# Optimization experiments

Measured on AMD Instinct MI355X. Metric: run time of the kernel, lower is better.

## Reference

```python
import jax, jax.numpy as jnp
import numpy as np

G, NP, DEG = 2, 332, 32            # graphs, ROIs per graph (AAL-332), out-degree
INDIM, D1, D2, D3, NCLASS = 332, 332, 332, 128, 2
KH, R = 6, 332                      # edge-weight-MLP bottleneck, ROI one-hot dim
K1, K2 = 166, 83                    # ceil(0.5*332), ceil(0.5*166)
N, E = G * NP, G * NP * DEG
NEG, EPS = -1e9, 1e-5


def _seg_softmax(logits, seg, n):
    m = jax.ops.segment_max(logits, seg, num_segments=n)
    e = jnp.exp(logits - m[seg])
    return e / jax.ops.segment_sum(e, seg, num_segments=n)[seg]


def _conv(xv, src, dst, eattr, emask, posv, W1, W2, nb, b, out_dim):
    # MyNNConv: per-node weight matrix from pos via tiny MLP, then
    # x' = x @ W_node, messages weighted by softmax(edge_weight) per target.
    n, din = xv.shape
    w = (jnp.maximum(posv @ W1, 0.0) @ W2 + nb).reshape(n, din, out_dim)
    xt = jnp.einsum('ni,nio->no', xv, w)
    sl = jnp.arange(n, dtype=src.dtype)                 # self loops, weight 1
    s2 = jnp.concatenate([src, sl])
    d2 = jnp.concatenate([dst, sl])
    logit = jnp.concatenate([jnp.where(emask, eattr, NEG), jnp.ones((n,), xv.dtype)])
    alpha = _seg_softmax(logit, d2, n)
    return jax.ops.segment_sum(alpha[:, None] * xt[s2], d2, num_segments=n) + b


def _pool(xv, src, dst, emask, w, g, n_per, k):
    # TopKPooling(multiplier=1, nonlinearity=sigmoid)
    score = jax.nn.sigmoid((xv @ w) / jnp.linalg.norm(w))
    _, idx = jax.lax.top_k(score.reshape(g, n_per), k)
    perm = (idx + jnp.arange(g)[:, None] * n_per).reshape(-1)
    x_new = xv[perm] * score[perm][:, None]
    newidx = jnp.full((g * n_per,), -1, jnp.int32).at[perm].set(jnp.arange(g * k, dtype=jnp.int32))
    ns, nd = newidx[src], newidx[dst]
    m = emask & (ns >= 0) & (nd >= 0)                   # edges with both ends kept
    return x_new, jnp.where(m, ns, 0), jnp.where(m, nd, 0), m, perm


def _readout(xv, seg, g, cnt):
    mx = jax.ops.segment_max(xv, seg, num_segments=g)
    mn = jax.ops.segment_sum(xv, seg, num_segments=g) / cnt
    return jnp.concatenate([mx, mn], axis=1)


def _bn(xv, gm, bt):
    return (xv - xv.mean(0)) / jnp.sqrt(xv.var(0) + EPS) * gm + bt


def _forward(edge_index, x, edge_attr, pos,
             conv1_W1, conv1_W2, conv1_nb, conv1_b, pool1_w,
             conv2_W1, conv2_W2, conv2_nb, conv2_b, pool2_w,
             fc1_W, fc1_b, bn1_g, bn1_b, fc2_W, fc2_b, bn2_g, bn2_b, fc3_W, fc3_b):
    src, dst = edge_index[0], edge_index[1]
    emask = jnp.ones((E,), bool)
    h = _conv(x, src, dst, edge_attr, emask, pos, conv1_W1, conv1_W2, conv1_nb, conv1_b, D1)
    h, src, dst, emask, perm1 = _pool(h, src, dst, emask, pool1_w, G, NP, K1)
    pos = pos[perm1]
    seg1 = jnp.repeat(jnp.arange(G, dtype=jnp.int32), K1)
    x1 = _readout(h, seg1, G, float(K1))
    h = _conv(h, src, dst, edge_attr, emask, pos, conv2_W1, conv2_W2, conv2_nb, conv2_b, D2)
    h, src, dst, emask, perm2 = _pool(h, src, dst, emask, pool2_w, G, K1, K2)
    seg2 = jnp.repeat(jnp.arange(G, dtype=jnp.int32), K2)
    x2 = _readout(h, seg2, G, float(K2))
    z = jnp.concatenate([x1, x2], axis=1)               # [G, (D1+D2)*2]
    z = jnp.maximum(_bn(z @ fc1_W + fc1_b, bn1_g, bn1_b), 0.0)
    z = jnp.maximum(_bn(z @ fc2_W + fc2_b, bn2_g, bn2_b), 0.0)
    return z @ fc3_W + fc3_b


def setup_inputs():
    key = jax.random.key(0)
    ks = jax.random.split(key, 16)
    rng = np.random.default_rng(0)
    src = np.repeat(np.arange(N), DEG)
    dst = rng.integers(0, NP, size=E) + (src // NP) * NP  # within-graph edges
    edge_index = jnp.asarray(np.stack([src, dst]), dtype=jnp.int32)
    batch = jnp.repeat(jnp.arange(G, dtype=jnp.int32), NP)
    pos = jnp.tile(jnp.eye(R, dtype=jnp.float32), (G, 1))  # ROI one-hot identity

    def lin(k, shape):
        return (jax.random.normal(k, shape, jnp.float32) / np.sqrt(shape[0])).astype(jnp.float32)

    return {
        'x': jax.random.normal(ks[0], (N, INDIM), jnp.float32),
        'edge_index': edge_index,
        'batch': batch,
        'edge_attr': jax.random.uniform(ks[1], (E,), jnp.float32),
        'pos': pos,
        'pheno': jax.random.normal(ks[2], (G, 16), jnp.float32),
        'conv1_W1': lin(ks[3], (R, KH)),
        'conv1_W2': lin(ks[4], (KH, INDIM * D1)),
        'conv1_nb': jnp.zeros((INDIM * D1,), jnp.float32),
        'conv1_b': jnp.zeros((D1,), jnp.float32),
        'pool1_w': lin(ks[5], (D1,)),
        'conv2_W1': lin(ks[6], (R, KH)),
        'conv2_W2': lin(ks[7], (KH, D1 * D2)),
        'conv2_nb': jnp.zeros((D1 * D2,), jnp.float32),
        'conv2_b': jnp.zeros((D2,), jnp.float32),
        'pool2_w': lin(ks[8], (D2,)),
        'fc1_W': lin(ks[9], ((D1 + D2) * 2, D2)),
        'fc1_b': jnp.zeros((D2,), jnp.float32),
        'bn1_g': jnp.ones((D2,), jnp.float32),
        'bn1_b': jnp.zeros((D2,), jnp.float32),
        'fc2_W': lin(ks[10], (D2, D3)),
        'fc2_b': jnp.zeros((D3,), jnp.float32),
        'bn2_g': jnp.ones((D3,), jnp.float32),
        'bn2_b': jnp.zeros((D3,), jnp.float32),
        'fc3_W': lin(ks[11], (D3, NCLASS)),
        'fc3_b': jnp.zeros((NCLASS,), jnp.float32),
    }


def reference(x, edge_index, batch, edge_attr, pos, pheno,
              conv1_W1, conv1_W2, conv1_nb, conv1_b, pool1_w,
              conv2_W1, conv2_W2, conv2_nb, conv2_b, pool2_w,
              fc1_W, fc1_b, bn1_g, bn1_b, fc2_W, fc2_b, bn2_g, bn2_b, fc3_W, fc3_b):
    return _forward(edge_index, x, edge_attr, pos,
                    conv1_W1, conv1_W2, conv1_nb, conv1_b, pool1_w,
                    conv2_W1, conv2_W2, conv2_nb, conv2_b, pool2_w,
                    fc1_W, fc1_b, bn1_g, bn1_b, fc2_W, fc2_b, bn2_g, bn2_b, fc3_W, fc3_b)
```

## Files before the change

### kernel.cpp

```cpp
#include <hip/hip_runtime.h>
#include <hip/hip_bf16.h>
#include <math.h>

#define GG 2
#define NPG 332
#define NN 664
#define EE 21248
#define EPG 10624
#define KHD 6
#define KP1 166
#define KP2 83
#define DIM 332
#define DD3 128
#define MAXIN 128
#define KTOT 2324
#define W2ROWS 1992
#define PLD 336
#define PROWS 704

__global__ void k_bucket1(const int* __restrict__ dst, int* __restrict__ cnt, int* __restrict__ bucket) {
    __shared__ int lcnt[NPG];
    int g = blockIdx.x, t = threadIdx.x;
    for (int i = t; i < NPG; i += 384) lcnt[i] = 0;
    __syncthreads();
    int e0 = g * EPG;
    for (int e = e0 + t; e < e0 + EPG; e += 384) {
        int dl = dst[e] - g * NPG;
        int slot = atomicAdd(&lcnt[dl], 1);
        if (slot < MAXIN) bucket[(size_t)(g * NPG + dl) * MAXIN + slot] = e;
    }
    __syncthreads();
    for (int i = t; i < NPG; i += 384) cnt[g * NPG + i] = lcnt[i];
}

#define BM 64
#define BN 64
#define BK 16
#define SPLITK 16

__global__ __launch_bounds__(256) void k_gemm(const float* __restrict__ X,
                                              const int* __restrict__ perm,
                                              const float* __restrict__ W1,
                                              const float* __restrict__ W2,
                                              const float* __restrict__ nb,
                                              float* __restrict__ P, int M) {
    __shared__ float As[BK][BM + 4];
    __shared__ float Bs[BK][BN];
    __shared__ float hs[BM][8];
    int tid = threadIdx.x;
    int tx = tid & 15, ty = tid >> 4;
    int col0 = blockIdx.x * BN, row0 = blockIdx.y * BM;
    if (tid < BM) {
        int r = row0 + tid;
        int roi = (r < M) ? ((perm ? perm[r] : r) % DIM) : 0;
        bool ok = r < M;
#pragma unroll
        for (int k = 0; k < 6; ++k)
            hs[tid][k] = ok ? fmaxf(W1[roi * KHD + k], 0.f) : 0.f;
        hs[tid][6] = ok ? 1.f : 0.f;
        hs[tid][7] = 0.f;
    }
    const int kc = (KTOT + SPLITK - 1) / SPLITK;
    int k0 = blockIdx.z * kc;
    int k1 = k0 + kc; if (k1 > KTOT) k1 = KTOT;
    __syncthreads();

    int kkA = tid & 15;
    int m0A = tid >> 4;
    int nB  = tid & 63;
    int kB0 = tid >> 6;

    float aReg[4], bReg[4];
    auto loadAB = [&](int kb) {
        {
            int kg = kb + kkA;
            bool kok = kg < k1;
            int kch = kg / DIM;
            int i = kg - kch * DIM;
#pragma unroll
            for (int mi = 0; mi < 4; ++mi) {
                int mm = m0A + mi * 16;
                int r = row0 + mm;
                aReg[mi] = (kok && r < M) ? hs[mm][kch] * X[(size_t)r * DIM + i] : 0.f;
            }
        }
        {
            int c = col0 + nB;
#pragma unroll
            for (int ki = 0; ki < 4; ++ki) {
                int r = kb + kB0 + ki * 4;
                float v = 0.f;
                if (r < k1 && c < DIM) {
                    const float* Brow = (r < W2ROWS) ? (W2 + (size_t)r * DIM)
                                                     : (nb + (size_t)(r - W2ROWS) * DIM);
                    v = Brow[c];
                }
                bReg[ki] = v;
            }
        }
    };
    auto writeAB = [&]() {
#pragma unroll
        for (int mi = 0; mi < 4; ++mi) As[kkA][m0A + mi * 16] = aReg[mi];
#pragma unroll
        for (int ki = 0; ki < 4; ++ki) Bs[kB0 + ki * 4][nB] = bReg[ki];
    };

    float acc[4][4] = {};
    loadAB(k0);
    writeAB();
    __syncthreads();
    for (int kb = k0; kb < k1; kb += BK) {
        int kn = kb + BK;
        bool more = kn < k1;
        if (more) loadAB(kn);
#pragma unroll
        for (int kk = 0; kk < BK; ++kk) {
            float a[4], b[4];
#pragma unroll
            for (int i = 0; i < 4; ++i) a[i] = As[kk][ty * 4 + i];
#pragma unroll
            for (int j = 0; j < 4; ++j) b[j] = Bs[kk][tx * 4 + j];
#pragma unroll
            for (int i = 0; i < 4; ++i)
#pragma unroll
                for (int j = 0; j < 4; ++j) acc[i][j] += a[i] * b[j];
        }
        __syncthreads();
        if (more) {
            writeAB();
            __syncthreads();
        }
    }
    int c0 = col0 + tx * 4;
    float* Pz = P + (size_t)blockIdx.z * PROWS * PLD;
#pragma unroll
    for (int i = 0; i < 4; ++i) {
        int r = row0 + ty * 4 + i;
        if (r < M) {
            float* dstp = Pz + (size_t)r * PLD + c0;
            if (c0 + 3 < DIM) {
                float4 v = make_float4(acc[i][0], acc[i][1], acc[i][2], acc[i][3]);
                *reinterpret_cast<float4*>(dstp) = v;
            } else {
#pragma unroll
                for (int j = 0; j < 4; ++j)
                    if (c0 + j < DIM) dstp[j] = acc[i][j];
            }
        }
    }
}

__global__ void k_reduce(const float* __restrict__ P, float* __restrict__ xt, int M) {
    int idx = blockIdx.x * 256 + threadIdx.x;
    if (idx >= M * DIM) return;
    int r = idx / DIM, o = idx - r * DIM;
    const float* p = P + (size_t)r * PLD + o;
    float s = 0.f;
#pragma unroll
    for (int z = 0; z < SPLITK; ++z) s += p[(size_t)z * PROWS * PLD];
    xt[idx] = s;
}

__global__ void k_agg(const float* __restrict__ xt, const int* __restrict__ cnt,
                      const int* __restrict__ bucket, const int* __restrict__ srcArr,
                      const float* __restrict__ eattr, const int* __restrict__ newidx,
                      const float* __restrict__ bias, const float* __restrict__ w,
                      float* __restrict__ out, float* __restrict__ score) {
    __shared__ float alpha[MAXIN];
    __shared__ int sidx[MAXIN];
    __shared__ float red[256];
    __shared__ float red2[256];
    int n = blockIdx.x, t = threadIdx.x;
    int c = cnt[n]; if (c > MAXIN) c = MAXIN;
    float mysum = 0.f;
    for (int j = t; j < c; j += 256) {
        int e = bucket[(size_t)n * MAXIN + j];
        int s = srcArr[e];
        if (newidx) s = newidx[s];
        float ex = expf(eattr[e]);
        alpha[j] = ex;
        sidx[j] = s;
        mysum += ex;
    }
    red[t] = mysum;
    __syncthreads();
    for (int off = 128; off > 0; off >>= 1) {
        if (t < off) red[t] += red[t + off];
        __syncthreads();
    }
    const float eself = 2.718281828459045f;
    float inv = 1.f / (red[0] + eself);
    __syncthreads();
    for (int j = t; j < c; j += 256) alpha[j] *= inv;
    __syncthreads();
    float aself = eself * inv;
    float dotp = 0.f, wsq = 0.f;
    for (int o = t; o < DIM; o += 256) {
        float acc = bias[o] + aself * xt[(size_t)n * DIM + o];
        for (int j = 0; j < c; ++j) acc += alpha[j] * xt[(size_t)sidx[j] * DIM + o];
        out[(size_t)n * DIM + o] = acc;
        float wv = w[o];
        dotp += acc * wv;
        wsq += wv * wv;
    }
    red[t] = dotp; red2[t] = wsq;
    __syncthreads();
    for (int off = 128; off > 0; off >>= 1) {
        if (t < off) { red[t] += red[t + off]; red2[t] += red2[t + off]; }
        __syncthreads();
    }
    if (t == 0) score[n] = 1.f / (1.f + expf(-red[0] / sqrtf(red2[0])));
}

__global__ void k_topk(const float* __restrict__ score, int n_per, int k,
                       int* __restrict__ perm, int* __restrict__ newidx,
                       const int* __restrict__ src, const int* __restrict__ dst,
                       int* __restrict__ cnt2, int* __restrict__ bucket2,
                       float* __restrict__ fz1, int fn1,
                       float* __restrict__ fz2, int fn2) {
    __shared__ float s[NPG];
    __shared__ short nidxS[NPG];
    int g = blockIdx.x, t = threadIdx.x;
    for (int i = t; i < n_per; i += 384) s[i] = score[g * n_per + i];
    if (cnt2) for (int i = t; i < k; i += 384) cnt2[g * k + i] = 0;
    if (fz1) for (int i = g * 384 + t; i < fn1; i += GG * 384) fz1[i] = 0.f;
    if (fz2) for (int i = g * 384 + t; i < fn2; i += GG * 384) fz2[i] = 0.f;
    __syncthreads();
    for (int i = t; i < n_per; i += 384) {
        float si = s[i];
        int r = 0;
        for (int j = 0; j < n_per; ++j) {
            float sj = s[j];
            r += (sj > si) || (sj == si && j < i);
        }
        int node = g * n_per + i;
        if (r < k) {
            perm[g * k + r] = node;
            newidx[node] = g * k + r;
            nidxS[i] = (short)(g * k + r);
        } else {
            newidx[node] = -1;
            nidxS[i] = -1;
        }
    }
    if (cnt2) {
        __syncthreads();
        int e0 = g * EPG;
        for (int e = e0 + t; e < e0 + EPG; e += 384) {
            int ns = nidxS[src[e] - g * n_per];
            int nd = nidxS[dst[e] - g * n_per];
            if (ns >= 0 && nd >= 0) {
                int slot = atomicAdd(&cnt2[nd], 1);
                if (slot < MAXIN) bucket2[(size_t)nd * MAXIN + slot] = e;
            }
        }
    }
}

__global__ void k_gather(const float* __restrict__ xv, const float* __restrict__ score,
                         const int* __restrict__ perm, int k,
                         float* __restrict__ xnew, float* __restrict__ z, int zbase) {
    __shared__ int   pS[KP1];
    __shared__ float sS[KP1];
    __shared__ float mxs[4][64];
    __shared__ float sms[4][64];
    int g = blockIdx.y;
    int t = threadIdx.x;
    for (int i = t; i < k; i += 256) {
        int p = perm[g * k + i];
        pS[i] = p;
        sS[i] = score[p];
    }
    __syncthreads();
    int oc = t & 63, rl = t >> 6;
    int o = blockIdx.x * 64 + oc;
    float mx = -3.4e38f, sm = 0.f;
    if (o < DIM) {
        int r = rl;
        for (; r + 4 < k; r += 8) {
            float v0 = xv[(size_t)pS[r] * DIM + o] * sS[r];
            float v1 = xv[(size_t)pS[r + 4] * DIM + o] * sS[r + 4];
            if (xnew) {
                xnew[(size_t)(g * k + r) * DIM + o] = v0;
                xnew[(size_t)(g * k + r + 4) * DIM + o] = v1;
            }
            mx = fmaxf(mx, fmaxf(v0, v1));
            sm += v0 + v1;
        }
        for (; r < k; r += 4) {
            float v = xv[(size_t)pS[r] * DIM + o] * sS[r];
            if (xnew) xnew[(size_t)(g * k + r) * DIM + o] = v;
            mx = fmaxf(mx, v);
            sm += v;
        }
    }
    mxs[rl][oc] = mx;
    sms[rl][oc] = sm;
    __syncthreads();
    if (rl == 0 && o < DIM) {
        float M = fmaxf(fmaxf(mxs[0][oc], mxs[1][oc]), fmaxf(mxs[2][oc], mxs[3][oc]));
        float S = sms[0][oc] + sms[1][oc] + sms[2][oc] + sms[3][oc];
        z[(size_t)g * 1328 + zbase + o] = M;
        z[(size_t)g * 1328 + zbase + DIM + o] = S / (float)k;
    }
}

__global__ void k_fc1(const float* __restrict__ z, const float* __restrict__ W,
                      float* __restrict__ hacc) {
    __shared__ float zs[2][166];
    int t = threadIdx.x;
    int j = blockIdx.x * 128 + t;
    int i0 = blockIdx.y * 166;
    for (int i = t; i < 166; i += 128) {
        zs[0][i] = z[i0 + i];
        zs[1][i] = z[1328 + i0 + i];
    }
    __syncthreads();
    if (j >= DIM) return;
    float a0 = 0.f, a1 = 0.f;
    for (int i = 0; i < 166; ++i) {
        float wv = W[(size_t)(i0 + i) * DIM + j];
        a0 += zs[0][i] * wv;
        a1 += zs[1][i] * wv;
    }
    atomicAdd(&hacc[j], a0);
    atomicAdd(&hacc[DIM + j], a1);
}

__global__ void k_fc2(const float* __restrict__ hacc, const float* __restrict__ fc1b,
                      const float* __restrict__ bn1g, const float* __restrict__ bn1b,
                      const float* __restrict__ W, float* __restrict__ f2acc) {
    __shared__ float z1s[2][83];
    int t = threadIdx.x;
    int i0 = blockIdx.x * 83;
    if (t < 83) {
        int col = i0 + t;
        float a0 = hacc[col] + fc1b[col];
        float a1 = hacc[DIM + col] + fc1b[col];
        float m = 0.5f * (a0 + a1);
        float d0 = a0 - m, d1 = a1 - m;
        float v = 0.5f * (d0 * d0 + d1 * d1);
        float is = 1.f / sqrtf(v + 1e-5f);
        float gj = bn1g[col], bj = bn1b[col];
        z1s[0][t] = fmaxf(d0 * is * gj + bj, 0.f);
        z1s[1][t] = fmaxf(d1 * is * gj + bj, 0.f);
    }
    __syncthreads();
    float a0 = 0.f, a1 = 0.f;
    for (int i = 0; i < 83; ++i) {
        float wv = W[(size_t)(i0 + i) * DD3 + t];
        a0 += z1s[0][i] * wv;
        a1 += z1s[1][i] * wv;
    }
    atomicAdd(&f2acc[t], a0);
    atomicAdd(&f2acc[DD3 + t], a1);
}

__global__ void k_head3(const float* __restrict__ f2acc, const float* __restrict__ fc2b,
                        const float* __restrict__ bn2g, const float* __restrict__ bn2b,
                        const float* __restrict__ fc3W, const float* __restrict__ fc3b,
                        float* __restrict__ out) {
    __shared__ float z2s[2][DD3];
    int t = threadIdx.x;
    {
        float a0 = f2acc[t] + fc2b[t];
        float a1 = f2acc[DD3 + t] + fc2b[t];
        float m = 0.5f * (a0 + a1);
        float d0 = a0 - m, d1 = a1 - m;
        float v = 0.5f * (d0 * d0 + d1 * d1);
        float is = 1.f / sqrtf(v + 1e-5f);
        float gj = bn2g[t], bj = bn2b[t];
        z2s[0][t] = fmaxf(d0 * is * gj + bj, 0.f);
        z2s[1][t] = fmaxf(d1 * is * gj + bj, 0.f);
    }
    __syncthreads();
    if (t < 4) {
        int g = t >> 1, c = t & 1;
        float acc = fc3b[c];
        for (int i = 0; i < DD3; ++i) acc += z2s[g][i] * fc3W[i * 2 + c];
        out[g * 2 + c] = acc;
    }
}

extern "C" void kernel_launch(void* const* d_in, const int* in_sizes, int n_in,
                              void* d_out, int out_size, void* d_ws, size_t ws_size,
                              hipStream_t stream) {
    (void)in_sizes; (void)n_in; (void)out_size; (void)ws_size;
    const float* x     = (const float*)d_in[0];
    const int*   eidx  = (const int*)d_in[1];
    const float* eattr = (const float*)d_in[3];
    const float* c1W1  = (const float*)d_in[6];
    const float* c1W2  = (const float*)d_in[7];
    const float* c1nb  = (const float*)d_in[8];
    const float* c1b   = (const float*)d_in[9];
    const float* p1w   = (const float*)d_in[10];
    const float* c2W1  = (const float*)d_in[11];
    const float* c2W2  = (const float*)d_in[12];
    const float* c2nb  = (const float*)d_in[13];
    const float* c2b   = (const float*)d_in[14];
    const float* p2w   = (const float*)d_in[15];
    const float* fc1W  = (const float*)d_in[16];
    const float* fc1b  = (const float*)d_in[17];
    const float* bn1g  = (const float*)d_in[18];
    const float* bn1b  = (const float*)d_in[19];
    const float* fc2W  = (const float*)d_in[20];
    const float* fc2b  = (const float*)d_in[21];
    const float* bn2g  = (const float*)d_in[22];
    const float* bn2b  = (const float*)d_in[23];
    const float* fc3W  = (const float*)d_in[24];
    const float* fc3b  = (const float*)d_in[25];

    const int* src = eidx;
    const int* dst = eidx + EE;

    char* w = (char*)d_ws;
    auto alloc = [&](size_t bytes) { void* p = (void*)w; w += ((bytes + 255) / 256) * 256; return p; };
    float* Pbuf    = (float*)alloc((size_t)SPLITK * PROWS * PLD * 4);
    int*   cnt1    = (int*)alloc(NN * 4);
    int*   bucket1 = (int*)alloc((size_t)NN * MAXIN * 4);
    float* xt1     = (float*)alloc((size_t)NN * DIM * 4);
    float* out1    = (float*)alloc((size_t)NN * DIM * 4);
    float* score1  = (float*)alloc(NN * 4);
    int*   perm1   = (int*)alloc(GG * KP1 * 4);
    int*   newidx1 = (int*)alloc(NN * 4);
    float* x1p     = (float*)alloc((size_t)GG * KP1 * DIM * 4);
    float* zbuf    = (float*)alloc(GG * 1328 * 4);
    int*   cnt2    = (int*)alloc(GG * KP1 * 4);
    int*   bucket2 = (int*)alloc((size_t)GG * KP1 * MAXIN * 4);
    float* xt2     = (float*)alloc((size_t)GG * KP1 * DIM * 4);
    float* out2    = (float*)alloc((size_t)GG * KP1 * DIM * 4);
    float* score2  = (float*)alloc(GG * KP1 * 4);
    int*   perm2   = (int*)alloc(GG * KP2 * 4);
    int*   newidx2 = (int*)alloc(GG * KP1 * 4);
    float* hacc    = (float*)alloc(2 * DIM * 4);
    float* f2acc   = (float*)alloc(2 * DD3 * 4);

    k_bucket1<<<GG, 384, 0, stream>>>(dst, cnt1, bucket1);
    k_gemm<<<dim3(6, 11, SPLITK), 256, 0, stream>>>(x, nullptr, c1W1, c1W2, c1nb, Pbuf, NN);
    k_reduce<<<(NN * DIM + 255) / 256, 256, 0, stream>>>(Pbuf, xt1, NN);
    k_agg<<<NN, 256, 0, stream>>>(xt1, cnt1, bucket1, src, eattr, nullptr, c1b, p1w, out1, score1);

    k_topk<<<GG, 384, 0, stream>>>(score1, NPG, KP1, perm1, newidx1,
                                   src, dst, cnt2, bucket2,
                                   nullptr, 0, nullptr, 0);
    k_gather<<<dim3(6, GG), 256, 0, stream>>>(out1, score1, perm1, KP1, x1p, zbuf, 0);

    k_gemm<<<dim3(6, 6, SPLITK), 256, 0, stream>>>(x1p, perm1, c2W1, c2W2, c2nb, Pbuf, GG * KP1);
    k_reduce<<<(GG * KP1 * DIM + 255) / 256, 256, 0, stream>>>(Pbuf, xt2, GG * KP1);
    k_agg<<<GG * KP1, 256, 0, stream>>>(xt2, cnt2, bucket2, src, eattr, newidx1, c2b, p2w, out2, score2);

    k_topk<<<GG, 384, 0, stream>>>(score2, KP1, KP2, perm2, newidx2,
                                   nullptr, nullptr, nullptr, nullptr,
                                   hacc, 2 * DIM, f2acc, 2 * DD3);
    k_gather<<<dim3(6, GG), 256, 0, stream>>>(out2, score2, perm2, KP2, nullptr, zbuf, 664);

    k_fc1<<<dim3(3, 8), 128, 0, stream>>>(zbuf, fc1W, hacc);
    k_fc2<<<4, 128, 0, stream>>>(hacc, fc1b, bn1g, bn1b, fc2W, f2acc);
    k_head3<<<1, 128, 0, stream>>>(f2acc, fc2b, bn2g, bn2b, fc3W, fc3b, (float*)d_out);
}
```

Measured before the change: 286.8 us.

## Fuse pool gather into conv2 GEMM, vectorise reduce, unroll agg, merge head kernels

The second GEMM now reads pooled rows straight from out1 through perm and folds the pool score into the per-row hidden coefficients, so the x1p intermediate is never written. The split-K reduce uses float4 loads and stores, and the aggregation inner loop runs four independent accumulators for more memory parallelism. fc2 and the final head are merged into one single-block kernel, removing a launch and the f2acc atomics, but fc2 then runs serially over 332 inputs in one block.

```diff
diff --git a/kernel.cpp b/kernel.cpp
--- a/kernel.cpp
+++ b/kernel.cpp
@@ -40,6 +40,7 @@
 
 __global__ __launch_bounds__(256) void k_gemm(const float* __restrict__ X,
                                               const int* __restrict__ perm,
+                                              const float* __restrict__ sc,
                                               const float* __restrict__ W1,
                                               const float* __restrict__ W2,
                                               const float* __restrict__ nb,
@@ -47,18 +48,22 @@
     __shared__ float As[BK][BM + 4];
     __shared__ float Bs[BK][BN];
     __shared__ float hs[BM][8];
+    __shared__ int   rowS[BM];
     int tid = threadIdx.x;
     int tx = tid & 15, ty = tid >> 4;
     int col0 = blockIdx.x * BN, row0 = blockIdx.y * BM;
     if (tid < BM) {
         int r = row0 + tid;
-        int roi = (r < M) ? ((perm ? perm[r] : r) % DIM) : 0;
         bool ok = r < M;
+        int prow = ok ? (perm ? perm[r] : r) : 0;
+        int roi = prow % DIM;
+        float s = (ok && sc) ? sc[prow] : 1.f;
 #pragma unroll
         for (int k = 0; k < 6; ++k)
-            hs[tid][k] = ok ? fmaxf(W1[roi * KHD + k], 0.f) : 0.f;
-        hs[tid][6] = ok ? 1.f : 0.f;
+            hs[tid][k] = ok ? fmaxf(W1[roi * KHD + k], 0.f) * s : 0.f;
+        hs[tid][6] = ok ? s : 0.f;
         hs[tid][7] = 0.f;
+        rowS[tid] = prow;
     }
     const int kc = (KTOT + SPLITK - 1) / SPLITK;
     int k0 = blockIdx.z * kc;
@@ -81,7 +86,7 @@
             for (int mi = 0; mi < 4; ++mi) {
                 int mm = m0A + mi * 16;
                 int r = row0 + mm;
-                aReg[mi] = (kok && r < M) ? hs[mm][kch] * X[(size_t)r * DIM + i] : 0.f;
+                aReg[mi] = (kok && r < M) ? hs[mm][kch] * X[(size_t)rowS[mm] * DIM + i] : 0.f;
             }
         }
         {
@@ -153,13 +158,17 @@
 
 __global__ void k_reduce(const float* __restrict__ P, float* __restrict__ xt, int M) {
     int idx = blockIdx.x * 256 + threadIdx.x;
-    if (idx >= M * DIM) return;
-    int r = idx / DIM, o = idx - r * DIM;
-    const float* p = P + (size_t)r * PLD + o;
-    float s = 0.f;
-#pragma unroll
-    for (int z = 0; z < SPLITK; ++z) s += p[(size_t)z * PROWS * PLD];
-    xt[idx] = s;
+    int tot = M * (DIM / 4);
+    if (idx >= tot) return;
+    int r = idx / (DIM / 4), o4 = idx - r * (DIM / 4);
+    const float* base = P + (size_t)r * PLD + o4 * 4;
+    float4 s = make_float4(0.f, 0.f, 0.f, 0.f);
+#pragma unroll
+    for (int z = 0; z < SPLITK; ++z) {
+        float4 v = *reinterpret_cast<const float4*>(base + (size_t)z * PROWS * PLD);
+        s.x += v.x; s.y += v.y; s.z += v.z; s.w += v.w;
+    }
+    *reinterpret_cast<float4*>(xt + (size_t)r * DIM + o4 * 4) = s;
 }
 
 __global__ void k_agg(const float* __restrict__ xt, const int* __restrict__ cnt,
@@ -197,8 +206,16 @@
     float aself = eself * inv;
     float dotp = 0.f, wsq = 0.f;
     for (int o = t; o < DIM; o += 256) {
-        float acc = bias[o] + aself * xt[(size_t)n * DIM + o];
-        for (int j = 0; j < c; ++j) acc += alpha[j] * xt[(size_t)sidx[j] * DIM + o];
+        float a0 = 0.f, a1 = 0.f, a2 = 0.f, a3 = 0.f;
+        int j = 0;
+        for (; j + 3 < c; j += 4) {
+            a0 += alpha[j]     * xt[(size_t)sidx[j]     * DIM + o];
+            a1 += alpha[j + 1] * xt[(size_t)sidx[j + 1] * DIM + o];
+            a2 += alpha[j + 2] * xt[(size_t)sidx[j + 2] * DIM + o];
+            a3 += alpha[j + 3] * xt[(size_t)sidx[j + 3] * DIM + o];
+        }
+        for (; j < c; ++j) a0 += alpha[j] * xt[(size_t)sidx[j] * DIM + o];
+        float acc = bias[o] + aself * xt[(size_t)n * DIM + o] + ((a0 + a1) + (a2 + a3));
         out[(size_t)n * DIM + o] = acc;
         float wv = w[o];
         dotp += acc * wv;
@@ -217,15 +234,13 @@
                        int* __restrict__ perm, int* __restrict__ newidx,
                        const int* __restrict__ src, const int* __restrict__ dst,
                        int* __restrict__ cnt2, int* __restrict__ bucket2,
-                       float* __restrict__ fz1, int fn1,
-                       float* __restrict__ fz2, int fn2) {
+                       float* __restrict__ fz1, int fn1) {
     __shared__ float s[NPG];
     __shared__ short nidxS[NPG];
     int g = blockIdx.x, t = threadIdx.x;
     for (int i = t; i < n_per; i += 384) s[i] = score[g * n_per + i];
     if (cnt2) for (int i = t; i < k; i += 384) cnt2[g * k + i] = 0;
     if (fz1) for (int i = g * 384 + t; i < fn1; i += GG * 384) fz1[i] = 0.f;
-    if (fz2) for (int i = g * 384 + t; i < fn2; i += GG * 384) fz2[i] = 0.f;
     __syncthreads();
     for (int i = t; i < n_per; i += 384) {
         float si = s[i];
@@ -260,7 +275,7 @@
 
 __global__ void k_gather(const float* __restrict__ xv, const float* __restrict__ score,
                          const int* __restrict__ perm, int k,
-                         float* __restrict__ xnew, float* __restrict__ z, int zbase) {
+                         float* __restrict__ z, int zbase) {
     __shared__ int   pS[KP1];
     __shared__ float sS[KP1];
     __shared__ float mxs[4][64];
@@ -281,16 +296,11 @@
         for (; r + 4 < k; r += 8) {
             float v0 = xv[(size_t)pS[r] * DIM + o] * sS[r];
             float v1 = xv[(size_t)pS[r + 4] * DIM + o] * sS[r + 4];
-            if (xnew) {
-                xnew[(size_t)(g * k + r) * DIM + o] = v0;
-                xnew[(size_t)(g * k + r + 4) * DIM + o] = v1;
-            }
             mx = fmaxf(mx, fmaxf(v0, v1));
             sm += v0 + v1;
         }
         for (; r < k; r += 4) {
             float v = xv[(size_t)pS[r] * DIM + o] * sS[r];
-            if (xnew) xnew[(size_t)(g * k + r) * DIM + o] = v;
             mx = fmaxf(mx, v);
             sm += v;
         }
@@ -328,14 +338,16 @@
     atomicAdd(&hacc[DIM + j], a1);
 }
 
-__global__ void k_fc2(const float* __restrict__ hacc, const float* __restrict__ fc1b,
-                      const float* __restrict__ bn1g, const float* __restrict__ bn1b,
-                      const float* __restrict__ W, float* __restrict__ f2acc) {
-    __shared__ float z1s[2][83];
+__global__ void k_head2(const float* __restrict__ hacc, const float* __restrict__ fc1b,
+                        const float* __restrict__ bn1g, const float* __restrict__ bn1b,
+                        const float* __restrict__ fc2W, const float* __restrict__ fc2b,
+                        const float* __restrict__ bn2g, const float* __restrict__ bn2b,
+                        const float* __restrict__ fc3W, const float* __restrict__ fc3b,
+                        float* __restrict__ out) {
+    __shared__ float z1s[2][DIM];
+    __shared__ float z2s[2][DD3];
     int t = threadIdx.x;
-    int i0 = blockIdx.x * 83;
-    if (t < 83) {
-        int col = i0 + t;
+    for (int col = t; col < DIM; col += 256) {
         float a0 = hacc[col] + fc1b[col];
         float a1 = hacc[DIM + col] + fc1b[col];
         float m = 0.5f * (a0 + a1);
@@ -343,29 +355,17 @@
         float v = 0.5f * (d0 * d0 + d1 * d1);
         float is = 1.f / sqrtf(v + 1e-5f);
         float gj = bn1g[col], bj = bn1b[col];
-        z1s[0][t] = fmaxf(d0 * is * gj + bj, 0.f);
-        z1s[1][t] = fmaxf(d1 * is * gj + bj, 0.f);
-    }
-    __syncthreads();
-    float a0 = 0.f, a1 = 0.f;
-    for (int i = 0; i < 83; ++i) {
-        float wv = W[(size_t)(i0 + i) * DD3 + t];
-        a0 += z1s[0][i] * wv;
-        a1 += z1s[1][i] * wv;
-    }
-    atomicAdd(&f2acc[t], a0);
-    atomicAdd(&f2acc[DD3 + t], a1);
-}
-
-__global__ void k_head3(const float* __restrict__ f2acc, const float* __restrict__ fc2b,
-                        const float* __restrict__ bn2g, const float* __restrict__ bn2b,
-                        const float* __restrict__ fc3W, const float* __restrict__ fc3b,
-                        float* __restrict__ out) {
-    __shared__ float z2s[2][DD3];
-    int t = threadIdx.x;
-    {
-        float a0 = f2acc[t] + fc2b[t];
-        float a1 = f2acc[DD3 + t] + fc2b[t];
+        z1s[0][col] = fmaxf(d0 * is * gj + bj, 0.f);
+        z1s[1][col] = fmaxf(d1 * is * gj + bj, 0.f);
+    }
+    __syncthreads();
+    if (t < DD3) {
+        float a0 = fc2b[t], a1 = a0;
+        for (int i = 0; i < DIM; ++i) {
+            float wv = fc2W[(size_t)i * DD3 + t];
+            a0 += z1s[0][i] * wv;
+            a1 += z1s[1][i] * wv;
+        }
         float m = 0.5f * (a0 + a1);
         float d0 = a0 - m, d1 = a1 - m;
         float v = 0.5f * (d0 * d0 + d1 * d1);
@@ -424,7 +424,6 @@
     float* score1  = (float*)alloc(NN * 4);
     int*   perm1   = (int*)alloc(GG * KP1 * 4);
     int*   newidx1 = (int*)alloc(NN * 4);
-    float* x1p     = (float*)alloc((size_t)GG * KP1 * DIM * 4);
     float* zbuf    = (float*)alloc(GG * 1328 * 4);
     int*   cnt2    = (int*)alloc(GG * KP1 * 4);
     int*   bucket2 = (int*)alloc((size_t)GG * KP1 * MAXIN * 4);
@@ -434,28 +433,26 @@
     int*   perm2   = (int*)alloc(GG * KP2 * 4);
     int*   newidx2 = (int*)alloc(GG * KP1 * 4);
     float* hacc    = (float*)alloc(2 * DIM * 4);
-    float* f2acc   = (float*)alloc(2 * DD3 * 4);
 
     k_bucket1<<<GG, 384, 0, stream>>>(dst, cnt1, bucket1);
-    k_gemm<<<dim3(6, 11, SPLITK), 256, 0, stream>>>(x, nullptr, c1W1, c1W2, c1nb, Pbuf, NN);
-    k_reduce<<<(NN * DIM + 255) / 256, 256, 0, stream>>>(Pbuf, xt1, NN);
+    k_gemm<<<dim3(6, 11, SPLITK), 256, 0, stream>>>(x, nullptr, nullptr, c1W1, c1W2, c1nb, Pbuf, NN);
+    k_reduce<<<(NN * (DIM / 4) + 255) / 256, 256, 0, stream>>>(Pbuf, xt1, NN);
     k_agg<<<NN, 256, 0, stream>>>(xt1, cnt1, bucket1, src, eattr, nullptr, c1b, p1w, out1, score1);
 
     k_topk<<<GG, 384, 0, stream>>>(score1, NPG, KP1, perm1, newidx1,
-                                   src, dst, cnt2, bucket2,
-                                   nullptr, 0, nullptr, 0);
-    k_gather<<<dim3(6, GG), 256, 0, stream>>>(out1, score1, perm1, KP1, x1p, zbuf, 0);
-
-    k_gemm<<<dim3(6, 6, SPLITK), 256, 0, stream>>>(x1p, perm1, c2W1, c2W2, c2nb, Pbuf, GG * KP1);
-    k_reduce<<<(GG * KP1 * DIM + 255) / 256, 256, 0, stream>>>(Pbuf, xt2, GG * KP1);
+                                   src, dst, cnt2, bucket2, nullptr, 0);
+    k_gather<<<dim3(6, GG), 256, 0, stream>>>(out1, score1, perm1, KP1, zbuf, 0);
+
+    k_gemm<<<dim3(6, 6, SPLITK), 256, 0, stream>>>(out1, perm1, score1, c2W1, c2W2, c2nb, Pbuf, GG * KP1);
+    k_reduce<<<(GG * KP1 * (DIM / 4) + 255) / 256, 256, 0, stream>>>(Pbuf, xt2, GG * KP1);
     k_agg<<<GG * KP1, 256, 0, stream>>>(xt2, cnt2, bucket2, src, eattr, newidx1, c2b, p2w, out2, score2);
 
     k_topk<<<GG, 384, 0, stream>>>(score2, KP1, KP2, perm2, newidx2,
                                    nullptr, nullptr, nullptr, nullptr,
-                                   hacc, 2 * DIM, f2acc, 2 * DD3);
-    k_gather<<<dim3(6, GG), 256, 0, stream>>>(out2, score2, perm2, KP2, nullptr, zbuf, 664);
+                                   hacc, 2 * DIM);
+    k_gather<<<dim3(6, GG), 256, 0, stream>>>(out2, score2, perm2, KP2, zbuf, 664);
 
     k_fc1<<<dim3(3, 8), 128, 0, stream>>>(zbuf, fc1W, hacc);
-    k_fc2<<<4, 128, 0, stream>>>(hacc, fc1b, bn1g, bn1b, fc2W, f2acc);
-    k_head3<<<1, 128, 0, stream>>>(f2acc, fc2b, bn2g, bn2b, fc3W, fc3b, (float*)d_out);
-}
+    k_head2<<<1, 256, 0, stream>>>(hacc, fc1b, bn1g, bn1b, fc2W, fc2b,
+                                   bn2g, bn2b, fc3W, fc3b, (float*)d_out);
+}
```

New measurement: 307.3 us. 7.1% more time.
